# Performance work log

Hardware: AMD Instinct MI355X
Metric: run time of the kernel (lower is better)

Reference implementation:

```python
import jax, jax.numpy as jnp
import numpy as np

# Module constants derived from init kwargs:
# factor=3, indices_per_spike=64, index_maximum=19, border_pad=5
FACTOR = 3
IPS = 64            # indices_per_spike
INDEX_MAX = 19
BP = 5              # border_pad == width
CENTER = (INDEX_MAX + BP) * FACTOR          # 72
LO = CENTER - BP * FACTOR                   # 57
HI = CENTER + BP * FACTOR                   # 87
NEW_CENTER = LO                             # 57
ALIGNED_LEN = (IPS + 2 * BP) * FACTOR - 2 * BP * FACTOR  # 192


def setup_inputs() -> dict:
    key = jax.random.key(0)
    K, L = 500000, 220
    spikes_up = jax.random.normal(key, (K, L), dtype=jnp.float32)
    return {"spikes_up": spikes_up}


def reference(spikes_up):
    K, L = spikes_up.shape
    hi = min(HI, L)
    # per-row argmax in search window [LO, hi)
    window = spikes_up[:, LO:hi]                               # (K, hi-LO)
    local_peaks = jnp.argmax(window, axis=1)                   # (K,)
    index_max = local_peaks + LO
    starts = index_max - CENTER + BP * FACTOR                  # (K,)
    ends = starts + ALIGNED_LEN
    in_bounds = (starts >= 0) & (ends <= L)
    # shifted gather with clamped offsets
    safe_starts = jnp.clip(starts, 0, L - ALIGNED_LEN)
    offsets = jnp.arange(ALIGNED_LEN)
    all_indices = jnp.clip(safe_starts[:, None] + offsets[None, :], 0, L - 1)  # (K, 192)
    aligned = jnp.take_along_axis(spikes_up, all_indices, axis=1)              # (K, 192)
    # validity: peak must land exactly at NEW_CENTER and the slice in bounds
    at_center = jnp.argmax(aligned, axis=1) == NEW_CENTER
    valid = at_center & in_bounds
    removed_mask = ~valid
    # strided downsample (every FACTOR-th sample), invalid rows zeroed
    ds_idx = jnp.arange(IPS) * FACTOR
    downsampled = aligned[:, ds_idx]                           # (K, 64)
    spikes_final = jnp.where(valid[:, None], downsampled, jnp.zeros((), spikes_up.dtype))
    return spikes_final, removed_mask
```

## Files before the change

### kernel.cpp

```cpp
#include <hip/hip_runtime.h>
#include <cfloat>

#define LCOLS        220
#define WIN_LO       57
#define WIN_HI       86
#define ALIGNED_LEN_ 192
#define MAX_START    28
#define IPS_         64
#define NEW_CENTER_  57
#define TILE_ROWS    32
#define TILE_WORDS   (TILE_ROWS * LCOLS)

__device__ __forceinline__ void async_copy16(const float* gsrc, float* ldst) {
    __builtin_amdgcn_global_load_lds(
        (const __attribute__((address_space(1))) void*)gsrc,
        (__attribute__((address_space(3))) void*)ldst, 16, 0, 0);
}

__global__ __launch_bounds__(128) void peak_align_tile(
    const float* __restrict__ in,
    float* __restrict__ out_spikes,
    float* __restrict__ out_mask,
    int K)
{
    __shared__ __align__(16) float tile[TILE_WORDS];
    __shared__ int   spack[TILE_ROWS];
    __shared__ float pval[128];
    __shared__ int   pidx[128];
    __shared__ int   rpack[TILE_ROWS];

    const int t    = threadIdx.x;
    const int lane = t & 63;
    const int wave = t >> 6;
    const long long base = (long long)blockIdx.x * TILE_ROWS;
    const int rows = (int)(((long long)K - base) < TILE_ROWS ? (K - base) : TILE_ROWS);
    const float* src = in + base * LCOLS;

    const int bytes = rows * (LCOLS * 4);
    const int nfull = bytes >> 10;
    for (int it = wave; it < nfull; it += 2) {
        async_copy16(src + (it << 8) + lane * 4, &tile[it << 8]);
    }
    const int rem = bytes - (nfull << 10);
    if (t * 16 < rem) {
        const float4 v = *(const float4*)(src + (nfull << 8) + t * 4);
        *(float4*)&tile[(nfull << 8) + t * 4] = v;
    }
    __syncthreads();

    if (t < rows) {
        const float* row = &tile[t * LCOLS];
        float bv = -FLT_MAX; int bi = WIN_LO;
        #pragma unroll
        for (int j = 14; j <= 21; ++j) {
            const float4 q = *(const float4*)(row + (j << 2));
            const float qq[4] = {q.x, q.y, q.z, q.w};
            #pragma unroll
            for (int k = 0; k < 4; ++k) {
                const int c = (j << 2) + k;
                if (c >= WIN_LO && c <= WIN_HI && qq[k] > bv) { bv = qq[k]; bi = c; }
            }
        }
        const int  start = bi - WIN_LO;
        const bool in_b  = (start <= MAX_START);
        spack[t] = (in_b ? start : MAX_START) | (in_b ? (1 << 8) : 0);
    }
    __syncthreads();

    {
        const int r = t & 31;
        const int q = t >> 5;
        const int jlo = q * 14;
        const int jhi = (q == 3) ? 55 : jlo + 14;
        float av = -FLT_MAX; int ai = 0x7fffffff;
        if (r < rows) {
            const int s = spack[r] & 0xFF;
            const float* row = &tile[r * LCOLS];
            for (int j = jlo; j < jhi; ++j) {
                const float4 qv = *(const float4*)(row + (j << 2));
                const float qq[4] = {qv.x, qv.y, qv.z, qv.w};
                #pragma unroll
                for (int k = 0; k < 4; ++k) {
                    const int c = (j << 2) + k;
                    const bool inr = (unsigned)(c - s) < (unsigned)ALIGNED_LEN_;
                    if (inr && qq[k] > av) { av = qq[k]; ai = c; }
                }
            }
        }
        pval[t] = av; pidx[t] = ai;
    }
    __syncthreads();

    if (t < rows) {
        float av = pval[t];        int ai = pidx[t];
        #pragma unroll
        for (int q = 1; q < 4; ++q) {
            const float v2 = pval[q * 32 + t];
            const int   i2 = pidx[q * 32 + t];
            if (v2 > av || (v2 == av && i2 < ai)) { av = v2; ai = i2; }
        }
        const int  pk    = spack[t];
        const int  s     = pk & 0xFF;
        const bool in_b  = (pk >> 8) != 0;
        const bool valid = in_b && (ai == s + NEW_CENTER_);
        rpack[t] = s | (valid ? (1 << 30) : 0);
        out_mask[base + t] = valid ? 0.0f : 1.0f;
    }
    __syncthreads();

    #pragma unroll
    for (int i = 0; i < 16; ++i) {
        const int rr = wave * 16 + i;
        if (rr < rows) {
            const int pk = rpack[rr];
            const int s  = pk & 0xFF;
            const float v = tile[rr * LCOLS + s + 3 * lane];
            out_spikes[(base + rr) * IPS_ + lane] = (pk & (1 << 30)) ? v : 0.0f;
        }
    }
}

extern "C" void kernel_launch(void* const* d_in, const int* in_sizes, int n_in,
                              void* d_out, int out_size, void* d_ws, size_t ws_size,
                              hipStream_t stream) {
    const float* in = (const float*)d_in[0];
    const int K = in_sizes[0] / LCOLS;

    float* out_spikes = (float*)d_out;
    float* out_mask   = out_spikes + (long long)K * IPS_;

    const int grid = (K + TILE_ROWS - 1) / TILE_ROWS;
    hipLaunchKernelGGL(peak_align_tile, dim3(grid), dim3(128), 0, stream,
                       in, out_spikes, out_mask, K);
}
```

Baseline: 594.5 us.

## Assign four threads per row and reduce argmax with wave shuffles instead of LDS

Each row of the tile is now handled by a quad of four adjacent threads. The window argmax and the aligned argmax are each split across the quad and combined with xor shuffles, which removes the shared-memory staging arrays and three block-wide barriers. Each thread then writes 16 contiguous output values as float4 stores instead of scalar per-lane stores. The quad shuffle tie-breaking has to keep first-index argmax semantics, and the float4 stores rely on 16-byte alignment of the output rows.

```diff
diff --git a/kernel.cpp b/kernel.cpp
--- a/kernel.cpp
+++ b/kernel.cpp
@@ -7,7 +7,6 @@
 #define ALIGNED_LEN_ 192
 #define MAX_START    28
 #define IPS_         64
-#define NEW_CENTER_  57
 #define TILE_ROWS    32
 #define TILE_WORDS   (TILE_ROWS * LCOLS)
 
@@ -23,11 +22,7 @@
     float* __restrict__ out_mask,
     int K)
 {
-    __shared__ __align__(16) float tile[TILE_WORDS];
-    __shared__ int   spack[TILE_ROWS];
-    __shared__ float pval[128];
-    __shared__ int   pidx[128];
-    __shared__ int   rpack[TILE_ROWS];
+    __shared__ __align__(16) float tile[TILE_WORDS + 4];
 
     const int t    = threadIdx.x;
     const int lane = t & 63;
@@ -48,74 +43,75 @@
     }
     __syncthreads();
 
-    if (t < rows) {
-        const float* row = &tile[t * LCOLS];
-        float bv = -FLT_MAX; int bi = WIN_LO;
+    const int r = t >> 2;
+    const int q = t & 3;
+    const bool live = (r < rows);
+    const float* row = &tile[r * LCOLS];
+
+    float bv = -FLT_MAX; int bi = 0x7fffffff;
+    if (live) {
         #pragma unroll
-        for (int j = 14; j <= 21; ++j) {
-            const float4 q = *(const float4*)(row + (j << 2));
-            const float qq[4] = {q.x, q.y, q.z, q.w};
+        for (int jj = 0; jj < 2; ++jj) {
+            const int j = 14 + 2 * q + jj;
+            const float4 v = *(const float4*)(row + (j << 2));
+            const float qq[4] = {v.x, v.y, v.z, v.w};
             #pragma unroll
             for (int k = 0; k < 4; ++k) {
                 const int c = (j << 2) + k;
                 if (c >= WIN_LO && c <= WIN_HI && qq[k] > bv) { bv = qq[k]; bi = c; }
             }
         }
-        const int  start = bi - WIN_LO;
-        const bool in_b  = (start <= MAX_START);
-        spack[t] = (in_b ? start : MAX_START) | (in_b ? (1 << 8) : 0);
     }
-    __syncthreads();
+    #pragma unroll
+    for (int m = 1; m <= 2; m <<= 1) {
+        const float ov = __shfl_xor(bv, m);
+        const int   oi = __shfl_xor(bi, m);
+        if (ov > bv || (ov == bv && oi < bi)) { bv = ov; bi = oi; }
+    }
+    const int  start = bi - WIN_LO;
+    const bool in_b  = (start <= MAX_START);
+    const int  s     = in_b ? start : MAX_START;
 
-    {
-        const int r = t & 31;
-        const int q = t >> 5;
-        const int jlo = q * 14;
-        const int jhi = (q == 3) ? 55 : jlo + 14;
-        float av = -FLT_MAX; int ai = 0x7fffffff;
-        if (r < rows) {
-            const int s = spack[r] & 0xFF;
-            const float* row = &tile[r * LCOLS];
-            for (int j = jlo; j < jhi; ++j) {
-                const float4 qv = *(const float4*)(row + (j << 2));
-                const float qq[4] = {qv.x, qv.y, qv.z, qv.w};
-                #pragma unroll
-                for (int k = 0; k < 4; ++k) {
-                    const int c = (j << 2) + k;
-                    const bool inr = (unsigned)(c - s) < (unsigned)ALIGNED_LEN_;
-                    if (inr && qq[k] > av) { av = qq[k]; ai = c; }
-                }
+    float av = -FLT_MAX; int ai = 0x7fffffff;
+    if (live) {
+        const int jlo = 14 * q;
+        #pragma unroll
+        for (int jj = 0; jj < 14; ++jj) {
+            const int j = jlo + jj;
+            const float4 v = *(const float4*)(row + (j << 2));
+            const float qq[4] = {v.x, v.y, v.z, v.w};
+            #pragma unroll
+            for (int k = 0; k < 4; ++k) {
+                const int c = (j << 2) + k;
+                const bool inr = (unsigned)(c - s) < (unsigned)ALIGNED_LEN_;
+                if (inr && qq[k] > av) { av = qq[k]; ai = c; }
             }
         }
-        pval[t] = av; pidx[t] = ai;
     }
-    __syncthreads();
+    #pragma unroll
+    for (int m = 1; m <= 2; m <<= 1) {
+        const float ov = __shfl_xor(av, m);
+        const int   oi = __shfl_xor(ai, m);
+        if (ov > av || (ov == av && oi < ai)) { av = ov; ai = oi; }
+    }
+    const bool valid = in_b && (ai == s + WIN_LO);
 
-    if (t < rows) {
-        float av = pval[t];        int ai = pidx[t];
+    if (live && q == 0) {
+        out_mask[base + r] = valid ? 0.0f : 1.0f;
+    }
+
+    if (live) {
+        const int cbase = s + 3 * (q << 4);
+        float4* dst = (float4*)&out_spikes[(base + r) * IPS_ + (q << 4)];
         #pragma unroll
-        for (int q = 1; q < 4; ++q) {
-            const float v2 = pval[q * 32 + t];
-            const int   i2 = pidx[q * 32 + t];
-            if (v2 > av || (v2 == av && i2 < ai)) { av = v2; ai = i2; }
-        }
-        const int  pk    = spack[t];
-        const int  s     = pk & 0xFF;
-        const bool in_b  = (pk >> 8) != 0;
-        const bool valid = in_b && (ai == s + NEW_CENTER_);
-        rpack[t] = s | (valid ? (1 << 30) : 0);
-        out_mask[base + t] = valid ? 0.0f : 1.0f;
-    }
-    __syncthreads();
-
-    #pragma unroll
-    for (int i = 0; i < 16; ++i) {
-        const int rr = wave * 16 + i;
-        if (rr < rows) {
-            const int pk = rpack[rr];
-            const int s  = pk & 0xFF;
-            const float v = tile[rr * LCOLS + s + 3 * lane];
-            out_spikes[(base + rr) * IPS_ + lane] = (pk & (1 << 30)) ? v : 0.0f;
+        for (int ii = 0; ii < 4; ++ii) {
+            float vv[4];
+            #pragma unroll
+            for (int k = 0; k < 4; ++k) {
+                const float g = row[cbase + 3 * ((ii << 2) + k)];
+                vv[k] = valid ? g : 0.0f;
+            }
+            dst[ii] = make_float4(vv[0], vv[1], vv[2], vv[3]);
         }
     }
 }
```

New measurement: 591.1 us. Within noise of the previous version (-0.6%).
